# Kernel optimization log

Hardware: AMD Instinct MI355X
Metric: run time of the kernel (lower is better)

Reference implementation:

```python
import jax, jax.numpy as jnp
import numpy as np
import math

EMBED_DIM = 768
HIDDEN_DIM = 96
N_HEAD = 8
BATCH = 32
K_LEN = 512
Q_LEN = 512


def setup_inputs() -> dict:
    key = jax.random.key(0)
    k1, k2, k3, k4 = jax.random.split(key, 4)
    k = jax.random.normal(k1, (BATCH, K_LEN, EMBED_DIM), dtype=jnp.float32)
    q = jax.random.normal(k2, (BATCH, Q_LEN, EMBED_DIM), dtype=jnp.float32)
    # per-head projection weights, as in nn.Parameter(torch.FloatTensor(n_head, embed_dim, hidden_dim))
    w_kx = jax.random.normal(k3, (N_HEAD, EMBED_DIM, HIDDEN_DIM), dtype=jnp.float32) * (1.0 / math.sqrt(EMBED_DIM))
    w_qx = jax.random.normal(k4, (N_HEAD, EMBED_DIM, HIDDEN_DIM), dtype=jnp.float32) * (1.0 / math.sqrt(EMBED_DIM))
    return {"k": k, "q": q, "w_kx": w_kx, "w_qx": w_qx}


def reference(k, q, w_kx, w_qx):
    # scaled_dot_product variant of ABSA-PyTorch Attention.
    mb, k_len, _ = k.shape
    q_len = q.shape[1]
    hidden = w_kx.shape[-1]
    # per-head projections: [h, b, len, d]  (torch: repeat over heads + bmm)
    kx = jnp.einsum('bke,hed->hbkd', k, w_kx)
    qx = jnp.einsum('bqe,hed->hbqd', q, w_qx)
    # scores [h, b, q, k], scaled
    score = jnp.einsum('hbqd,hbkd->hbqk', qx, kx) / jnp.sqrt(jnp.asarray(hidden, kx.dtype))
    attn = jax.nn.softmax(score, axis=-1)
    # weighted sum over the PROJECTED keys (kx), as in the original: bmm(score, kx)
    out = jnp.einsum('hbqk,hbkd->hbqd', attn, kx)
    # torch.cat(torch.split(output, mb, dim=0), dim=-1): concat heads on last dim
    out = jnp.transpose(out, (1, 2, 0, 3)).reshape(mb, q_len, w_kx.shape[0] * hidden)
    return out
```

## Files before the change

### kernel.cpp

```cpp
#include <hip/hip_runtime.h>
#include <hip/hip_bf16.h>

typedef short short8 __attribute__((ext_vector_type(8)));
typedef short short4v __attribute__((ext_vector_type(4)));
typedef float floatx4 __attribute__((ext_vector_type(4)));

#define EMB 768
#define DH 96
#define NHEAD 8
#define NBATCH 32
#define SEQ 512
#define MROWS (NBATCH * SEQ)

__device__ __forceinline__ unsigned short f2bf(float x) {
    __hip_bfloat16 h = __float2bfloat16(x);
    union { __hip_bfloat16 b; unsigned short u; } c;
    c.b = h;
    return c.u;
}

__global__ __launch_bounds__(256) void cvt_w_kernel(
    const float* __restrict__ wk, const float* __restrict__ wq,
    unsigned short* __restrict__ wtk, unsigned short* __restrict__ wtq)
{
    __shared__ float ws[64][97];
    const int h = blockIdx.x, et = blockIdx.y;
    const float* wsrc = (blockIdx.z ? wq : wk) + (size_t)h * EMB * DH;
    unsigned short* o = blockIdx.z ? wtq : wtk;
    const int t = threadIdx.x;
    const int e0 = et * 64;
    #pragma unroll
    for (int i = 0; i < 6; ++i) {
        int f = i * 256 + t;
        int e = f / 24, c = f % 24;
        float4 v = *(const float4*)(wsrc + (size_t)(e0 + e) * DH + c * 4);
        ws[e][c*4+0] = v.x; ws[e][c*4+1] = v.y; ws[e][c*4+2] = v.z; ws[e][c*4+3] = v.w;
    }
    __syncthreads();
    #pragma unroll
    for (int i = 0; i < 3; ++i) {
        int f = i * 256 + t;
        int d = f >> 3, c8 = f & 7;
        short8 v;
        #pragma unroll
        for (int j = 0; j < 8; ++j) v[j] = (short)f2bf(ws[c8*8+j][d]);
        *(short8*)(o + (size_t)(h*DH + d) * EMB + e0 + c8*8) = v;
    }
}

__global__ __launch_bounds__(256, 2) void proj_kernel(
    const float* __restrict__ x,
    const unsigned short* __restrict__ wt,
    unsigned short* __restrict__ xp)
{
    __shared__ char As[16384];
    __shared__ char Bs[32768];
    const int t = threadIdx.x;
    const int wv = t >> 6, l = t & 63;
    const int lr = l & 15, lg = l >> 4, l7 = l & 7;
    const int mt = blockIdx.x * 128, nt = blockIdx.y * 256;
    const int mw = (wv >> 1) * 64, nw = (wv & 1) * 128;

    floatx4 acc[4][8];
    #pragma unroll
    for (int a = 0; a < 4; ++a)
        #pragma unroll
        for (int b = 0; b < 8; ++b) acc[a][b] = (floatx4){0.f, 0.f, 0.f, 0.f};

    for (int kt = 0; kt < EMB / 64; ++kt) {
        __syncthreads();
        #pragma unroll
        for (int i = 0; i < 4; ++i) {
            int f = i * 256 + t;
            int row = f >> 3, s = f & 7;
            const float* xs = x + (size_t)(mt + row) * EMB + kt*64 + s*8;
            float4 ga = *(const float4*)xs;
            float4 gb = *(const float4*)(xs + 4);
            union { unsigned short h[8]; short8 s8; } pk;
            pk.h[0] = f2bf(ga.x); pk.h[1] = f2bf(ga.y);
            pk.h[2] = f2bf(ga.z); pk.h[3] = f2bf(ga.w);
            pk.h[4] = f2bf(gb.x); pk.h[5] = f2bf(gb.y);
            pk.h[6] = f2bf(gb.z); pk.h[7] = f2bf(gb.w);
            *(short8*)(As + row*128 + ((s ^ (row & 7)) * 16)) = pk.s8;
        }
        #pragma unroll
        for (int i = 0; i < 8; ++i) {
            int f = i * 256 + t;
            int row = f >> 3, s = f & 7;
            short8 gw = *(const short8*)(wt + (size_t)(nt + row) * EMB + kt*64 + s*8);
            *(short8*)(Bs + row*128 + ((s ^ (row & 7)) * 16)) = gw;
        }
        __syncthreads();
        #pragma unroll
        for (int ks = 0; ks < 2; ++ks) {
            const int sl = (ks*4 + lg) ^ l7;
            short8 af[4], bf[8];
            #pragma unroll
            for (int mf = 0; mf < 4; ++mf)
                af[mf] = *(const short8*)(As + (mw + 16*mf + lr) * 128 + sl*16);
            #pragma unroll
            for (int nf = 0; nf < 8; ++nf)
                bf[nf] = *(const short8*)(Bs + (nw + 16*nf + lr) * 128 + sl*16);
            #pragma unroll
            for (int mf = 0; mf < 4; ++mf)
                #pragma unroll
                for (int nf = 0; nf < 8; ++nf)
                    acc[mf][nf] = __builtin_amdgcn_mfma_f32_16x16x32_bf16(
                        af[mf], bf[nf], acc[mf][nf], 0, 0, 0);
        }
    }
    #pragma unroll
    for (int mf = 0; mf < 4; ++mf)
        #pragma unroll
        for (int r = 0; r < 4; ++r) {
            int m = mt + mw + 16*mf + lg*4 + r;
            unsigned short* op = xp + (size_t)m * EMB + nt + nw + lr;
            #pragma unroll
            for (int nf = 0; nf < 8; ++nf) op[16*nf] = f2bf(acc[mf][nf][r]);
        }
}

__global__ __launch_bounds__(512) void attn_kernel(
    const unsigned short* __restrict__ kx,
    const unsigned short* __restrict__ qx,
    float* __restrict__ out)
{
    __shared__ char Ks[64 * 192];
    __shared__ char Kt2[16 * 768];
    const int t = threadIdx.x;
    const int wv = t >> 6, l = t & 63;
    const int lr = l & 15, lg = l >> 4;
    const int q0 = blockIdx.x * 256, b = blockIdx.y, h = blockIdx.z;
    const size_t bq = (size_t)b * SEQ;
    const int hcol = h * DH;
    const float scale = 0.10206207261596575f;

    short8 qf[2][3];
    #pragma unroll
    for (int mf = 0; mf < 2; ++mf)
        #pragma unroll
        for (int ks = 0; ks < 3; ++ks)
            qf[mf][ks] = *(const short8*)(qx
                + (bq + q0 + 32*wv + 16*mf + lr) * EMB + hcol + ks*32 + lg*8);

    floatx4 of[2][6];
    #pragma unroll
    for (int mf = 0; mf < 2; ++mf)
        #pragma unroll
        for (int dt = 0; dt < 6; ++dt) of[mf][dt] = (floatx4){0.f, 0.f, 0.f, 0.f};
    float lsum[2] = {0.f, 0.f};

    for (int kt = 0; kt < SEQ / 64; ++kt) {
        __syncthreads();
        if (t < 384) {
            int rp = t / 12, s = t - rp * 12;
            int r0 = rp * 2;
            const unsigned short* src = kx + (bq + kt*64 + r0) * EMB + hcol + s*8;
            short8 g0 = *(const short8*)src;
            short8 g1 = *(const short8*)(src + EMB);
            *(short8*)(Ks + r0*192 + ((s + r0) % 12) * 16) = g0;
            *(short8*)(Ks + (r0+1)*192 + ((s + r0 + 1) % 12) * 16) = g1;
            const int c = rp >> 1, tau = 5 * (c & 3);
            char* kb = Kt2 + c*768 + ((rp & 1) << 2);
            #pragma unroll
            for (int j = 0; j < 8; ++j) {
                int d = s*8 + j;
                unsigned int pr = (unsigned int)(unsigned short)g0[j]
                                | ((unsigned int)(unsigned short)g1[j] << 16);
                *(unsigned int*)(kb + ((d ^ tau) << 3)) = pr;
            }
        }
        __syncthreads();

        floatx4 sf[2][4];
        #pragma unroll
        for (int mf = 0; mf < 2; ++mf)
            #pragma unroll
            for (int nf = 0; nf < 4; ++nf) sf[mf][nf] = (floatx4){0.f, 0.f, 0.f, 0.f};
        #pragma unroll
        for (int ks = 0; ks < 3; ++ks) {
            short8 bk[4];
            #pragma unroll
            for (int nf = 0; nf < 4; ++nf) {
                int row = 16*nf + lr;
                bk[nf] = *(const short8*)(Ks + row*192 + ((ks*4 + lg + row) % 12) * 16);
            }
            #pragma unroll
            for (int mf = 0; mf < 2; ++mf)
                #pragma unroll
                for (int nf = 0; nf < 4; ++nf)
                    sf[mf][nf] = __builtin_amdgcn_mfma_f32_16x16x32_bf16(
                        bk[nf], qf[mf][ks], sf[mf][nf], 0, 0, 0);
        }

        #pragma unroll
        for (int mf = 0; mf < 2; ++mf)
            #pragma unroll
            for (int nf = 0; nf < 4; ++nf)
                #pragma unroll
                for (int r = 0; r < 4; ++r) {
                    float p = __expf(fmaf(sf[mf][nf][r], scale, -12.0f));
                    sf[mf][nf][r] = p;
                    lsum[mf] += p;
                }

        #pragma unroll
        for (int ks2 = 0; ks2 < 2; ++ks2) {
            union { unsigned short hsh[8]; short8 s8; } ap[2];
            #pragma unroll
            for (int mf = 0; mf < 2; ++mf)
                #pragma unroll
                for (int j = 0; j < 8; ++j)
                    ap[mf].hsh[j] = f2bf(sf[mf][2*ks2 + (j >> 2)][j & 3]);
            const int cbase = (8*ks2 + lg) * 768;
            const int tau = 5 * lg;
            #pragma unroll
            for (int dt = 0; dt < 6; ++dt) {
                const int gofs = ((16*dt + lr) ^ tau) << 3;
                short4v lo = *(const short4v*)(Kt2 + cbase + gofs);
                short4v hi = *(const short4v*)(Kt2 + cbase + 3072 + gofs);
                short8 bv;
                bv[0] = lo[0]; bv[1] = lo[1]; bv[2] = lo[2]; bv[3] = lo[3];
                bv[4] = hi[0]; bv[5] = hi[1]; bv[6] = hi[2]; bv[7] = hi[3];
                #pragma unroll
                for (int mf = 0; mf < 2; ++mf)
                    of[mf][dt] = __builtin_amdgcn_mfma_f32_16x16x32_bf16(
                        ap[mf].s8, bv, of[mf][dt], 0, 0, 0);
            }
        }
    }

    float invq[2];
    #pragma unroll
    for (int mf = 0; mf < 2; ++mf) {
        float v = lsum[mf];
        v += __shfl_xor(v, 16);
        v += __shfl_xor(v, 32);
        invq[mf] = 1.0f / v;
    }
    #pragma unroll
    for (int mf = 0; mf < 2; ++mf)
        #pragma unroll
        for (int r = 0; r < 4; ++r) {
            float inv = __shfl(invq[mf], 4*lg + r);
            int q = q0 + 32*wv + 16*mf + 4*lg + r;
            float* op = out + (bq + q) * (NHEAD*DH) + hcol + lr;
            #pragma unroll
            for (int dt = 0; dt < 6; ++dt) op[16*dt] = of[mf][dt][r] * inv;
        }
}

extern "C" void kernel_launch(void* const* d_in, const int* in_sizes, int n_in,
                              void* d_out, int out_size, void* d_ws, size_t ws_size,
                              hipStream_t stream) {
    const float* kin = (const float*)d_in[0];
    const float* qin = (const float*)d_in[1];
    const float* wk  = (const float*)d_in[2];
    const float* wq  = (const float*)d_in[3];
    float* out = (float*)d_out;

    unsigned short* wsu = (unsigned short*)d_ws;
    const size_t SZX = (size_t)MROWS * EMB;
    unsigned short* kxb = wsu;
    unsigned short* qxb = wsu + SZX;
    unsigned short* wtk = wsu + 2*SZX;
    unsigned short* wtq = wtk + (size_t)EMB * (NHEAD*DH);

    cvt_w_kernel<<<dim3(NHEAD, EMB/64, 2), 256, 0, stream>>>(wk, wq, wtk, wtq);
    proj_kernel<<<dim3(MROWS/128, (NHEAD*DH)/256), 256, 0, stream>>>(kin, wtk, kxb);
    proj_kernel<<<dim3(MROWS/128, (NHEAD*DH)/256), 256, 0, stream>>>(qin, wtq, qxb);
    attn_kernel<<<dim3(SEQ/256, NBATCH, NHEAD), 512, 0, stream>>>(kxb, qxb, out);
}
```

Baseline: 119.1 us.

## Double-buffer K tiles in LDS and prefetch next tile into registers

The attention kernel now keeps two LDS buffers for the K tile and its transposed copy, and alternates between them across iterations. Each iteration prefetches the next K tile from global memory into registers after the barrier, so the load overlaps with the MFMA work. One of the two barriers per iteration goes away. In exchange, LDS use doubles to about 48KB per block, which may reduce occupancy, and holding the prefetched data adds register pressure.

Measured after the change: 115.6 us. -2.9%, faster.

```diff
diff --git a/kernel.cpp b/kernel.cpp
--- a/kernel.cpp
+++ b/kernel.cpp
@@ -125,8 +125,8 @@
     const unsigned short* __restrict__ qx,
     float* __restrict__ out)
 {
-    __shared__ char Ks[64 * 192];
-    __shared__ char Kt2[16 * 768];
+    __shared__ char KsB[2 * 12288];
+    __shared__ char KtB[2 * 12288];
     const int t = threadIdx.x;
     const int wv = t >> 6, l = t & 63;
     const int lr = l & 15, lg = l >> 4;
@@ -135,6 +135,10 @@
     const int hcol = h * DH;
     const float scale = 0.10206207261596575f;
 
+    const bool stv = (t < 384);
+    const int rp = t / 12, ss = t - rp * 12;
+    const int r0 = rp * 2;
+
     short8 qf[2][3];
     #pragma unroll
     for (int mf = 0; mf < 2; ++mf)
@@ -150,28 +154,41 @@
         for (int dt = 0; dt < 6; ++dt) of[mf][dt] = (floatx4){0.f, 0.f, 0.f, 0.f};
     float lsum[2] = {0.f, 0.f};
 
+    short8 pg0, pg1;
+    if (stv) {
+        const unsigned short* src = kx + (bq + r0) * EMB + hcol + ss*8;
+        pg0 = *(const short8*)src;
+        pg1 = *(const short8*)(src + EMB);
+    }
+
+    int cur = 0;
     for (int kt = 0; kt < SEQ / 64; ++kt) {
-        __syncthreads();
-        if (t < 384) {
-            int rp = t / 12, s = t - rp * 12;
-            int r0 = rp * 2;
-            const unsigned short* src = kx + (bq + kt*64 + r0) * EMB + hcol + s*8;
-            short8 g0 = *(const short8*)src;
-            short8 g1 = *(const short8*)(src + EMB);
-            *(short8*)(Ks + r0*192 + ((s + r0) % 12) * 16) = g0;
-            *(short8*)(Ks + (r0+1)*192 + ((s + r0 + 1) % 12) * 16) = g1;
+        if (stv) {
+            char* Kc = KsB + cur * 12288;
+            char* Tc = KtB + cur * 12288;
+            *(short8*)(Kc + r0*192 + ((ss + r0) % 12) * 16) = pg0;
+            *(short8*)(Kc + (r0+1)*192 + ((ss + r0 + 1) % 12) * 16) = pg1;
             const int c = rp >> 1, tau = 5 * (c & 3);
-            char* kb = Kt2 + c*768 + ((rp & 1) << 2);
+            char* kb = Tc + c*768 + ((rp & 1) << 2);
             #pragma unroll
             for (int j = 0; j < 8; ++j) {
-                int d = s*8 + j;
-                unsigned int pr = (unsigned int)(unsigned short)g0[j]
-                                | ((unsigned int)(unsigned short)g1[j] << 16);
+                int d = ss*8 + j;
+                unsigned int pr = (unsigned int)(unsigned short)pg0[j]
+                                | ((unsigned int)(unsigned short)pg1[j] << 16);
                 *(unsigned int*)(kb + ((d ^ tau) << 3)) = pr;
             }
         }
         __syncthreads();
 
+        if (kt < SEQ/64 - 1 && stv) {
+            const unsigned short* src = kx + (bq + (kt+1)*64 + r0) * EMB + hcol + ss*8;
+            pg0 = *(const short8*)src;
+            pg1 = *(const short8*)(src + EMB);
+        }
+
+        const char* Kc = KsB + cur * 12288;
+        const char* Tc = KtB + cur * 12288;
+
         floatx4 sf[2][4];
         #pragma unroll
         for (int mf = 0; mf < 2; ++mf)
@@ -183,7 +200,7 @@
             #pragma unroll
             for (int nf = 0; nf < 4; ++nf) {
                 int row = 16*nf + lr;
-                bk[nf] = *(const short8*)(Ks + row*192 + ((ks*4 + lg + row) % 12) * 16);
+                bk[nf] = *(const short8*)(Kc + row*192 + ((ks*4 + lg + row) % 12) * 16);
             }
             #pragma unroll
             for (int mf = 0; mf < 2; ++mf)
@@ -217,8 +234,8 @@
             #pragma unroll
             for (int dt = 0; dt < 6; ++dt) {
                 const int gofs = ((16*dt + lr) ^ tau) << 3;
-                short4v lo = *(const short4v*)(Kt2 + cbase + gofs);
-                short4v hi = *(const short4v*)(Kt2 + cbase + 3072 + gofs);
+                short4v lo = *(const short4v*)(Tc + cbase + gofs);
+                short4v hi = *(const short4v*)(Tc + cbase + 3072 + gofs);
                 short8 bv;
                 bv[0] = lo[0]; bv[1] = lo[1]; bv[2] = lo[2]; bv[3] = lo[3];
                 bv[4] = hi[0]; bv[5] = hi[1]; bv[6] = hi[2]; bv[7] = hi[3];
@@ -228,6 +245,7 @@
                         ap[mf].s8, bv, of[mf][dt], 0, 0, 0);
             }
         }
+        cur ^= 1;
     }
 
     float invq[2];
```
